# Performance work log

Measured on AMD Instinct MI355X. Metric: run time of the kernel, lower is better.

Reference implementation:

```python
import math
import jax, jax.numpy as jnp
import numpy as np

B, L, ENC_IN, TFEAT = 32, 1024, 21, 4
DM, EXP = 256, 2
DI = DM * EXP            # 512 d_inner
DST = 64                 # d_state (= configs.d_ff in this repo)
HD = 64                  # headdim
NH = DI // HD            # 8 heads
DC = 4                   # d_conv
NL = 4                   # n_layers
PRED = 192
CO = 21
Q = 64                   # SSD chunk length
DIP = 2 * DI + 2 * DST + NH    # in_proj out dim (z, xBC, dt)
CONVD = DI + 2 * DST           # depthwise-conv channels


def silu(x):
    return x * jax.nn.sigmoid(x)


def positional_embedding(l, d):
    pe = np.zeros((l, d), np.float32)
    pos = np.arange(l, dtype=np.float32)[:, None]
    div = np.exp(np.arange(0, d, 2, dtype=np.float32) * (-math.log(10000.0) / d))
    pe[:, 0::2] = np.sin(pos * div)
    pe[:, 1::2] = np.cos(pos * div)
    return jnp.asarray(pe)


def layernorm(x, g, b):
    m = jnp.mean(x, -1, keepdims=True)
    v = jnp.mean((x - m) ** 2, -1, keepdims=True)
    return (x - m) * jax.lax.rsqrt(v + 1e-5) * g + b


def segsum(x):
    # x: (..., T) -> (..., T, T); out[i,j] = sum_{j<k<=i} x[k], -inf above diagonal
    T = x.shape[-1]
    xx = jnp.broadcast_to(x[..., :, None], (*x.shape, T))
    m1 = jnp.tril(jnp.ones((T, T), bool), -1)
    xs = jnp.cumsum(jnp.where(m1, xx, 0.0), axis=-2)
    m2 = jnp.tril(jnp.ones((T, T), bool), 0)
    return jnp.where(m2, xs, -jnp.inf)


def ssd(X, A, Bm, Cm):
    # chunked SSD (Mamba2). X: (b,l,h,p) = x*dt; A: (b,l,h) = dt*(-exp(A_log)); B,C: (b,l,n)
    b, l, h, p = X.shape
    c = l // Q
    Xc = X.reshape(b, c, Q, h, p)
    Ac = A.reshape(b, c, Q, h).transpose(0, 3, 1, 2)      # (b,h,c,q)
    Bc = Bm.reshape(b, c, Q, -1)
    Cc = Cm.reshape(b, c, Q, -1)
    Acum = jnp.cumsum(Ac, -1)                              # (b,h,c,q)
    Lmat = jnp.exp(segsum(Ac))                             # (b,h,c,q,q)
    Y_diag = jnp.einsum('bcqn,bcsn,bhcqs,bcshp->bcqhp', Cc, Bc, Lmat, Xc)
    decay_states = jnp.exp(Acum[..., -1:] - Acum)          # (b,h,c,q)
    states = jnp.einsum('bcqn,bhcq,bcqhp->bchpn', Bc, decay_states, Xc)
    states = jnp.concatenate([jnp.zeros_like(states[:, :1]), states], axis=1)  # (b,c+1,h,p,n)
    decay_chunk = jnp.exp(segsum(jnp.pad(Acum[..., -1], ((0, 0), (0, 0), (1, 0)))))  # (b,h,c+1,c+1)
    new_states = jnp.einsum('bhzc,bchpn->bzhpn', decay_chunk, states)
    states = new_states[:, :-1]                            # (b,c,h,p,n) entering each chunk
    sdo = jnp.exp(Acum)                                    # (b,h,c,q)
    Y_off = jnp.einsum('bcqn,bchpn,bhcq->bcqhp', Cc, states, sdo)
    return (Y_diag + Y_off).reshape(b, l, h, p)


def mamba2(x, Wi, cw, cb, dtb, Alog, Dp, gw, Wo):
    b, l, _ = x.shape
    zxbcdt = x @ Wi.T                                      # (b,l,DIP)
    z = zxbcdt[..., :DI]
    xBC = zxbcdt[..., DI:DI + CONVD]
    dt = zxbcdt[..., DI + CONVD:]
    # causal depthwise conv (kernel DC) + SiLU
    xp = jnp.pad(xBC, ((0, 0), (DC - 1, 0), (0, 0)))
    xBC = silu(sum(xp[:, k:k + l, :] * cw[:, k] for k in range(DC)) + cb)
    xs = xBC[..., :DI].reshape(b, l, NH, HD)
    Bm = xBC[..., DI:DI + DST]
    Cm = xBC[..., DI + DST:]
    dt = jax.nn.softplus(dt + dtb)                         # (b,l,NH)
    A = -jnp.exp(Alog)                                     # (NH,)
    y = ssd(xs * dt[..., None], dt * A, Bm, Cm) + xs * Dp[:, None]
    y = y.reshape(b, l, DI)
    y = y * silu(z)                                        # gated RMSNorm
    y = y * jax.lax.rsqrt(jnp.mean(y * y, -1, keepdims=True) + 1e-5) * gw
    return y @ Wo.T


def setup_inputs():
    key = jax.random.key(0)
    ks = jax.random.split(key, 16)
    x_enc = jax.random.normal(ks[0], (B, L, ENC_IN), jnp.float32)
    x_mark_enc = jax.random.normal(ks[1], (B, L, TFEAT), jnp.float32)
    x_dec = jax.random.normal(ks[2], (B, 240, ENC_IN), jnp.float32)
    x_mark_dec = jax.random.normal(ks[3], (B, 240, TFEAT), jnp.float32)
    token_w = jax.random.normal(ks[4], (DM, ENC_IN, 3), jnp.float32) * 0.1
    temb_w = jax.random.normal(ks[5], (DM, TFEAT), jnp.float32) * 0.1
    ln_g = jnp.ones((NL, DM), jnp.float32)
    ln_b = jnp.zeros((NL, DM), jnp.float32)
    in_proj_w = jax.random.normal(ks[6], (NL, DIP, DM), jnp.float32) * (DM ** -0.5)
    conv_w = jax.random.normal(ks[7], (NL, CONVD, DC), jnp.float32) * 0.2
    conv_b = jnp.zeros((NL, CONVD), jnp.float32)
    dt_bias = jax.random.normal(ks[8], (NL, NH), jnp.float32) * 0.5
    A_log = jnp.log(jax.random.uniform(ks[9], (NL, NH), jnp.float32, 1.0, 16.0))
    Dskip = jnp.ones((NL, NH), jnp.float32)
    gnorm_w = jnp.ones((NL, DI), jnp.float32)
    out_proj_w = jax.random.normal(ks[10], (NL, DM, DI), jnp.float32) * (DI ** -0.5)
    head_w = jax.random.normal(ks[11], (CO, DM), jnp.float32) * (DM ** -0.5)
    return dict(x_enc=x_enc, x_mark_enc=x_mark_enc, x_dec=x_dec, x_mark_dec=x_mark_dec,
                token_w=token_w, temb_w=temb_w, ln_g=ln_g, ln_b=ln_b,
                in_proj_w=in_proj_w, conv_w=conv_w, conv_b=conv_b, dt_bias=dt_bias,
                A_log=A_log, Dskip=Dskip, gnorm_w=gnorm_w, out_proj_w=out_proj_w,
                head_w=head_w)


def reference(x_enc, x_mark_enc, x_dec, x_mark_dec, token_w, temb_w, ln_g, ln_b,
              in_proj_w, conv_w, conv_b, dt_bias, A_log, Dskip, gnorm_w, out_proj_w, head_w):
    # instance normalization (detached stats)
    mean = jax.lax.stop_gradient(jnp.mean(x_enc, 1, keepdims=True))
    xz = x_enc - mean
    std = jax.lax.stop_gradient(jnp.sqrt(jnp.var(xz, axis=1, keepdims=True) + 1e-5))
    xz = xz / std
    l = xz.shape[1]
    # token embedding: circular-pad Conv1d(enc_in->d_model, k=3)
    xpad = jnp.pad(xz, ((0, 0), (1, 1), (0, 0)), mode='wrap')
    tok = sum(jnp.einsum('blc,dc->bld', xpad[:, k:k + l], token_w[:, :, k]) for k in range(3))
    h = tok + positional_embedding(l, DM)[None] + x_mark_enc @ temb_w.T
    for i in range(NL):
        y = mamba2(h, in_proj_w[i], conv_w[i], conv_b[i], dt_bias[i], A_log[i],
                   Dskip[i], gnorm_w[i], out_proj_w[i])
        h = layernorm(h + y, ln_g[i], ln_b[i])
    out = h @ head_w.T
    out = out * std + mean
    return out[:, -PRED:, :]
```

## Files before the change

### kernel.cpp

```cpp
#include <hip/hip_runtime.h>
#include <hip/hip_bf16.h>


typedef unsigned short ushort_t;
typedef unsigned int uint_t;
typedef __attribute__((ext_vector_type(8))) short short8;
typedef __attribute__((ext_vector_type(4))) float f32x4;
typedef __attribute__((ext_vector_type(4))) ushort_t ushort4_t;

__device__ __forceinline__ float b2f(ushort_t u) {
    uint_t v = ((uint_t)u) << 16;
    return __builtin_bit_cast(float, v);
}
__device__ __forceinline__ ushort_t f2b(float f) {
    uint_t u = __builtin_bit_cast(uint_t, f);
    uint_t r = (u + 0x7FFFu + ((u >> 16) & 1u)) >> 16;
    return (ushort_t)r;
}
__device__ __forceinline__ float silu_f(float x) {
    return x / (1.f + __expf(-x));
}
__device__ __forceinline__ void gl_lds16(const ushort_t* g, ushort_t* l) {
    __builtin_amdgcn_global_load_lds(
        (const __attribute__((address_space(1))) unsigned int*)g,
        (__attribute__((address_space(3))) unsigned int*)l, 16, 0, 0);
}

__global__ __launch_bounds__(256) void cvt_pad_ip(const float* __restrict__ in,
        ushort_t* __restrict__ out) {
    int i = blockIdx.x * 256 + threadIdx.x;
    if (i >= 4 * 1280 * 256) return;
    int layer = i / (1280 * 256);
    int rem = i - layer * 1280 * 256;
    int n = rem >> 8, k = rem & 255;
    out[i] = (n < 1160) ? f2b(in[(size_t)layer * 1160 * 256 + n * 256 + k]) : (ushort_t)0;
}
__global__ __launch_bounds__(256) void cvt_wop(const float* __restrict__ in,
        const float* __restrict__ gw, ushort_t* __restrict__ out) {
    int i = blockIdx.x * 256 + threadIdx.x;
    int layer = i >> 17;
    int c = i & 511;
    out[i] = f2b(in[i] * gw[layer * 512 + c]);
}
__global__ __launch_bounds__(256) void cvt_convw(const float* __restrict__ in,
        float* __restrict__ out) {
    int i = blockIdx.x * 256 + threadIdx.x;
    if (i >= 10240) return;
    int layer = i / 2560;
    int rem = i - layer * 2560;
    int k = rem / 640, ch = rem - k * 640;
    out[i] = in[layer * 2560 + ch * 4 + k];
}

__global__ __launch_bounds__(256) void pe_kernel(float* __restrict__ pe) {
    int l = blockIdx.x, d = threadIdx.x;
    float div = __expf((float)(d & ~1) * (-9.210340371976184f / 256.0f));
    float arg = (float)l * div;
    pe[l * 256 + d] = (d & 1) ? cosf(arg) : sinf(arg);
}

__global__ __launch_bounds__(256) void stats_kernel(const float* __restrict__ xe,
        float* __restrict__ meanb, float* __restrict__ stdb, float* __restrict__ rstdb) {
    int bi = blockIdx.x;
    int b = bi / 21, c = bi - b * 21;
    int tid = threadIdx.x;
    float s = 0.f, s2 = 0.f;
    for (int l = tid; l < 1024; l += 256) {
        float v = xe[(b * 1024 + l) * 21 + c];
        s += v; s2 += v * v;
    }
    __shared__ float r1[4], r2[4];
    for (int o = 32; o > 0; o >>= 1) { s += __shfl_down(s, o, 64); s2 += __shfl_down(s2, o, 64); }
    if ((tid & 63) == 0) { r1[tid >> 6] = s; r2[tid >> 6] = s2; }
    __syncthreads();
    if (tid == 0) {
        float S = r1[0] + r1[1] + r1[2] + r1[3];
        float S2 = r2[0] + r2[1] + r2[2] + r2[3];
        float m = S * (1.f / 1024.f);
        float var = S2 * (1.f / 1024.f) - m * m;
        float sd = sqrtf(var + 1e-5f);
        meanb[bi] = m; stdb[bi] = sd; rstdb[bi] = 1.f / sd;
    }
}

__global__ __launch_bounds__(256) void embed3_kernel(const float* __restrict__ xe,
        const float* __restrict__ xm, const float* __restrict__ tokw,
        const float* __restrict__ tembw, const float* __restrict__ pe,
        const float* __restrict__ meanb, const float* __restrict__ rstdb,
        float* __restrict__ h, ushort_t* __restrict__ hbf) {
    int blk = blockIdx.x;
    int b = blk >> 4, t = blk & 15;
    int l0 = t * 64;
    int tid = threadIdx.x;
    __shared__ float xw[66][22];
    __shared__ float xmw[64][4];
    __shared__ float mn[21], rs[21];
    if (tid < 21) { mn[tid] = meanb[b * 21 + tid]; rs[tid] = rstdb[b * 21 + tid]; }
    float twr[63];
    {
        const float* tp = tokw + tid * 63;
        #pragma unroll
        for (int i = 0; i < 63; i++) twr[i] = tp[i];
    }
    float tbr[4];
    #pragma unroll
    for (int k = 0; k < 4; k++) tbr[k] = tembw[tid * 4 + k];
    __syncthreads();
    for (int i = tid; i < 1386; i += 256) {
        int row = i / 21, c = i - row * 21;
        int gl = (l0 - 1 + row + 1024) & 1023;
        xw[row][c] = (xe[(size_t)(b * 1024 + gl) * 21 + c] - mn[c]) * rs[c];
    }
    {
        int row = tid >> 2, c = tid & 3;
        xmw[row][c] = xm[(size_t)(b * 1024 + l0 + row) * 4 + c];
    }
    __syncthreads();
    int d = tid;
    float acc2 = 0.f, acc1 = 0.f;
    for (int r = 0; r < 66; r++) {
        float s0 = 0.f, s1 = 0.f, s2 = 0.f;
        #pragma unroll
        for (int c = 0; c < 21; c++) {
            float xv = xw[r][c];
            s0 += xv * twr[c * 3 + 0];
            s1 += xv * twr[c * 3 + 1];
            s2 += xv * twr[c * 3 + 2];
        }
        if (r >= 2) {
            int li = r - 2;
            float acc = acc2 + s2 + pe[(size_t)(l0 + li) * 256 + d];
            #pragma unroll
            for (int k = 0; k < 4; k++) acc += xmw[li][k] * tbr[k];
            size_t o = (size_t)(b * 1024 + l0 + li) * 256 + d;
            h[o] = acc;
            hbf[o] = f2b(acc);
        }
        acc2 = acc1 + s1;
        acc1 = s0;
    }
}

template<int KDIM>
__device__ __forceinline__ void gemm128_main(const ushort_t* __restrict__ Ab,
        const ushort_t* __restrict__ Wb, ushort_t* sA, ushort_t* sW,
        f32x4 (&acc)[16], int m0, int n0) {
    int tid = threadIdx.x;
    int w = tid >> 6, lane = tid & 63;
    int wm = w >> 1, wn = w & 1;
    int rr = lane & 15, quad = lane >> 4;
    int srow0 = w * 32 + (lane >> 2);
    int skk = (lane & 3) * 8;
    int sl0 = w * 1024 + lane * 8;
    for (int k0 = 0; k0 < KDIM; k0 += 64) {
        __syncthreads();
        #pragma unroll
        for (int p = 0; p < 2; p++) {
            #pragma unroll
            for (int j = 0; j < 2; j++) {
                int row = srow0 + j * 16;
                int koff = k0 + p * 32 + skk;
                gl_lds16(Ab + (size_t)(m0 + row) * KDIM + koff, &sA[p * 4096 + sl0 + j * 512]);
                gl_lds16(Wb + (size_t)(n0 + row) * KDIM + koff, &sW[p * 4096 + sl0 + j * 512]);
            }
        }
        __syncthreads();
        #pragma unroll
        for (int p = 0; p < 2; p++) {
            short8 a[4], b[4];
            #pragma unroll
            for (int i = 0; i < 4; i++)
                a[i] = *(const short8*)&sA[p * 4096 + (wm * 64 + i * 16 + rr) * 32 + quad * 8];
            #pragma unroll
            for (int j = 0; j < 4; j++)
                b[j] = *(const short8*)&sW[p * 4096 + (wn * 64 + j * 16 + rr) * 32 + quad * 8];
            #pragma unroll
            for (int i = 0; i < 4; i++)
                #pragma unroll
                for (int j = 0; j < 4; j++)
                    acc[i * 4 + j] = __builtin_amdgcn_mfma_f32_16x16x32_bf16(a[i], b[j], acc[i * 4 + j], 0, 0, 0);
        }
    }
}

__global__ __launch_bounds__(256) void gemm_ip(const ushort_t* __restrict__ A,
        const ushort_t* __restrict__ W, ushort_t* __restrict__ zbuf,
        ushort_t* __restrict__ xbuf) {
    int blk = blockIdx.x;
    int tm = blk / 10, tn = blk - tm * 10;
    int m0 = tm * 128, n0 = tn * 128;
    __shared__ ushort_t sA[8192], sW[8192];
    f32x4 acc[16];
    #pragma unroll
    for (int i = 0; i < 16; i++) acc[i] = (f32x4){0.f, 0.f, 0.f, 0.f};
    gemm128_main<256>(A, W, sA, sW, acc, m0, n0);
    int lane = threadIdx.x & 63, w = threadIdx.x >> 6;
    int wm = w >> 1, wn = w & 1;
    int rr = lane & 15, quad = lane >> 4;
    #pragma unroll
    for (int i = 0; i < 4; i++) {
        int mrow = m0 + wm * 64 + i * 16 + quad * 4;
        #pragma unroll
        for (int j = 0; j < 4; j++) {
            int n = n0 + wn * 64 + j * 16 + rr;
            #pragma unroll
            for (int r2 = 0; r2 < 4; r2++) {
                ushort_t v = f2b(acc[i * 4 + j][r2]);
                if (n < 512) zbuf[(size_t)(mrow + r2) * 512 + n] = v;
                else if (n < 1160) xbuf[(size_t)(mrow + r2) * 704 + (n - 512)] = v;
            }
        }
    }
}

__global__ __launch_bounds__(256) void gemm_og(const ushort_t* __restrict__ Yb,
        const ushort_t* __restrict__ Zb, const ushort_t* __restrict__ Wb,
        float* __restrict__ h, ushort_t* __restrict__ hbf,
        const float* __restrict__ lng, const float* __restrict__ lnb) {
    int m0 = blockIdx.x * 64;
    int tid = threadIdx.x;
    int w = tid >> 6, lane = tid & 63;
    int wm = w >> 1, wn = w & 1;
    int rr = lane & 15, quad = lane >> 4;
    __shared__ ushort_t sA[4096];
    __shared__ ushort_t sW[16384];
    __shared__ float gssq[64];
    __shared__ float rsum[64][2], rssq[64][2];

    int arow = tid >> 2;
    int akq = (tid & 3) * 16;
    const ushort_t* yrow = Yb + (size_t)(m0 + arow) * 512 + akq;
    const ushort_t* zrow = Zb + (size_t)(m0 + arow) * 512 + akq;
    ushort_t* adst = &sA[((tid & 3) >> 1) * 2048 + arow * 32 + (tid & 1) * 16];

    f32x4 acc[2][8];
    #pragma unroll
    for (int i = 0; i < 2; i++)
        #pragma unroll
        for (int j = 0; j < 8; j++) acc[i][j] = (f32x4){0.f, 0.f, 0.f, 0.f};
    float ssqr = 0.f;

    short8 y0 = *(const short8*)(yrow);
    short8 y1 = *(const short8*)(yrow + 8);
    short8 z0 = *(const short8*)(zrow);
    short8 z1 = *(const short8*)(zrow + 8);

    for (int k0 = 0; k0 < 512; k0 += 64) {
        __syncthreads();
        short8 ga, gb;
        #pragma unroll
        for (int jj = 0; jj < 8; jj++) {
            float g = b2f(((ushort_t*)&y0)[jj]) * silu_f(b2f(((ushort_t*)&z0)[jj]));
            ssqr += g * g;
            ((ushort_t*)&ga)[jj] = f2b(g);
        }
        #pragma unroll
        for (int jj = 0; jj < 8; jj++) {
            float g = b2f(((ushort_t*)&y1)[jj]) * silu_f(b2f(((ushort_t*)&z1)[jj]));
            ssqr += g * g;
            ((ushort_t*)&gb)[jj] = f2b(g);
        }
        *(short8*)adst = ga;
        *(short8*)(adst + 8) = gb;
        if (k0 + 64 < 512) {
            y0 = *(const short8*)(yrow + k0 + 64);
            y1 = *(const short8*)(yrow + k0 + 72);
            z0 = *(const short8*)(zrow + k0 + 64);
            z1 = *(const short8*)(zrow + k0 + 72);
        }
        #pragma unroll
        for (int p = 0; p < 2; p++) {
            #pragma unroll
            for (int j = 0; j < 4; j++)
                gl_lds16(Wb + (size_t)(w * 64 + j * 16 + (lane >> 2)) * 512
                             + k0 + p * 32 + (lane & 3) * 8,
                         &sW[p * 8192 + w * 2048 + j * 512 + lane * 8]);
        }
        __syncthreads();
        #pragma unroll
        for (int p = 0; p < 2; p++) {
            short8 a[2], b[8];
            #pragma unroll
            for (int i = 0; i < 2; i++)
                a[i] = *(const short8*)&sA[p * 2048 + (wm * 32 + i * 16 + rr) * 32 + quad * 8];
            #pragma unroll
            for (int j = 0; j < 8; j++)
                b[j] = *(const short8*)&sW[p * 8192 + (wn * 128 + j * 16 + rr) * 32 + quad * 8];
            #pragma unroll
            for (int i = 0; i < 2; i++)
                #pragma unroll
                for (int j = 0; j < 8; j++)
                    acc[i][j] = __builtin_amdgcn_mfma_f32_16x16x32_bf16(a[i], b[j], acc[i][j], 0, 0, 0);
        }
    }

    ssqr += __shfl_xor(ssqr, 1, 64);
    ssqr += __shfl_xor(ssqr, 2, 64);
    if ((tid & 3) == 0) gssq[arow] = ssqr;
    __syncthreads();

    float gl[8], bl[8];
    #pragma unroll
    for (int j = 0; j < 8; j++) {
        int col = wn * 128 + j * 16 + rr;
        gl[j] = lng[col]; bl[j] = lnb[col];
    }
    #pragma unroll
    for (int i = 0; i < 2; i++) {
        #pragma unroll
        for (int r2 = 0; r2 < 4; r2++) {
            int rowl = wm * 32 + i * 16 + quad * 4 + r2;
            float rmsv = rsqrtf(gssq[rowl] * (1.f / 512.f) + 1e-5f);
            size_t gbase = (size_t)(m0 + rowl) * 256;
            float s = 0.f, s2 = 0.f;
            #pragma unroll
            for (int j = 0; j < 8; j++) {
                int col = wn * 128 + j * 16 + rr;
                float xv = h[gbase + col] + acc[i][j][r2] * rmsv;
                acc[i][j][r2] = xv;
                s += xv; s2 += xv * xv;
            }
            #pragma unroll
            for (int o = 1; o < 16; o <<= 1) {
                s += __shfl_xor(s, o, 64);
                s2 += __shfl_xor(s2, o, 64);
            }
            if (rr == 0) { rsum[rowl][wn] = s; rssq[rowl][wn] = s2; }
        }
    }
    __syncthreads();
    #pragma unroll
    for (int i = 0; i < 2; i++) {
        #pragma unroll
        for (int r2 = 0; r2 < 4; r2++) {
            int rowl = wm * 32 + i * 16 + quad * 4 + r2;
            float S = rsum[rowl][0] + rsum[rowl][1];
            float S2 = rssq[rowl][0] + rssq[rowl][1];
            float mu = S * (1.f / 256.f);
            float var = S2 * (1.f / 256.f) - mu * mu;
            float rstd = rsqrtf(var + 1e-5f);
            size_t gbase = (size_t)(m0 + rowl) * 256;
            #pragma unroll
            for (int j = 0; j < 8; j++) {
                int col = wn * 128 + j * 16 + rr;
                float o = (acc[i][j][r2] - mu) * rstd * gl[j] + bl[j];
                h[gbase + col] = o;
                hbf[gbase + col] = f2b(o);
            }
        }
    }
}

__global__ __launch_bounds__(256) void conv_kernel(const ushort_t* __restrict__ xbuf,
        const float* __restrict__ cwt, const float* __restrict__ cb,
        const float* __restrict__ dtb, ushort_t* __restrict__ xc,
        float* __restrict__ dts) {
    if (blockIdx.x >= 2560) {
        int r = (blockIdx.x - 2560) * 256 + threadIdx.x;
        short8 dv = *(const short8*)(xbuf + (size_t)r * 704 + 640);
        #pragma unroll
        for (int j = 0; j < 8; j++) {
            float x = b2f(((ushort_t*)&dv)[j]) + dtb[j];
            dts[(size_t)r * 8 + j] = (x > 20.f) ? x : log1pf(__expf(x));
        }
        return;
    }
    int idx = blockIdx.x * 256 + threadIdx.x;
    int g = idx % 80;
    int rt = idx / 80;
    int ch0 = g * 8;
    int b = rt >> 8;
    int l0 = (rt & 255) << 2;
    float wgt[4][8];
    #pragma unroll
    for (int k = 0; k < 4; k++) {
        float4 w0 = *(const float4*)(cwt + k * 640 + ch0);
        float4 w1 = *(const float4*)(cwt + k * 640 + ch0 + 4);
        wgt[k][0] = w0.x; wgt[k][1] = w0.y; wgt[k][2] = w0.z; wgt[k][3] = w0.w;
        wgt[k][4] = w1.x; wgt[k][5] = w1.y; wgt[k][6] = w1.z; wgt[k][7] = w1.w;
    }
    float bias[8];
    {
        float4 b0 = *(const float4*)(cb + ch0);
        float4 b1 = *(const float4*)(cb + ch0 + 4);
        bias[0] = b0.x; bias[1] = b0.y; bias[2] = b0.z; bias[3] = b0.w;
        bias[4] = b1.x; bias[5] = b1.y; bias[6] = b1.z; bias[7] = b1.w;
    }
    short8 xr[7];
    const ushort_t* base = xbuf + (size_t)(b * 1024 + l0) * 704 + ch0;
    #pragma unroll
    for (int i = 0; i < 7; i++) {
        int ll = l0 - 3 + i;
        if (ll >= 0) xr[i] = *(const short8*)(base + (ptrdiff_t)(i - 3) * 704);
        else         xr[i] = (short8){0, 0, 0, 0, 0, 0, 0, 0};
    }
    #pragma unroll
    for (int lo = 0; lo < 4; lo++) {
        float acc[8];
        #pragma unroll
        for (int j = 0; j < 8; j++) acc[j] = bias[j];
        #pragma unroll
        for (int k = 0; k < 4; k++) {
            #pragma unroll
            for (int j = 0; j < 8; j++)
                acc[j] += b2f(((ushort_t*)&xr[lo + k])[j]) * wgt[k][j];
        }
        short8 o;
        #pragma unroll
        for (int j = 0; j < 8; j++) ((ushort_t*)&o)[j] = f2b(silu_f(acc[j]));
        *(short8*)(xc + (size_t)(b * 1024 + l0 + lo) * 640 + ch0) = o;
    }
}

__global__ __launch_bounds__(256) void ssd_stateA4(const ushort_t* __restrict__ xc,
        const float* __restrict__ dts, const float* __restrict__ alog,
        float* __restrict__ stbuf, float* __restrict__ acbuf) {
    int idx = blockIdx.x;
    int bh = idx >> 2, grp = idx & 3;
    int b = bh >> 3, h = bh & 7;
    float Ah = -__expf(alog[h]);
    int tid = threadIdx.x;
    int q = tid >> 2, pb = (tid & 3) * 16;
    int w = tid >> 6, lane = tid & 63;
    int rr = lane & 15, quad = lane >> 4, qb = w * 16;

    __shared__ ushort_t Bt[64][72], Xt[64][72];
    __shared__ float dec_s[64];
    __shared__ float ad_sh;

    float T[4][4];
    #pragma unroll
    for (int t = 0; t < 4; t++)
        #pragma unroll
        for (int r2 = 0; r2 < 4; r2++) T[t][r2] = 0.f;

    ushort_t bv[16], xv[16];
    float d_pf = 0.f;
    {
        int chunk = grp * 4;
        int l0 = chunk * 64;
        const ushort_t* xrow = xc + (size_t)(b * 1024 + l0 + q) * 640;
        *(short8*)&bv[0] = *(const short8*)(xrow + 512 + pb);
        *(short8*)&bv[8] = *(const short8*)(xrow + 512 + pb + 8);
        *(short8*)&xv[0] = *(const short8*)(xrow + h * 64 + pb);
        *(short8*)&xv[8] = *(const short8*)(xrow + h * 64 + pb + 8);
        if (tid < 64)
            d_pf = dts[(size_t)(b * 1024 + l0 + tid) * 8 + h];
    }

    for (int c4 = 0; c4 < 4; c4++) {
        int chunk = grp * 4 + c4;
        size_t cidx = (size_t)bh * 16 + chunk;
        #pragma unroll
        for (int j = 0; j < 16; j++) Xt[pb + j][q] = xv[j];
        if (tid < 64) {
            float d = d_pf;
            float a = d * Ah;
            #pragma unroll
            for (int off = 1; off < 64; off <<= 1) {
                float t = __shfl_up(a, off, 64);
                if (tid >= off) a += t;
            }
            acbuf[cidx * 64 + tid] = a;
            float tot = __shfl(a, 63, 64);
            dec_s[tid] = __expf(tot - a) * d;
            if (tid == 0) ad_sh = __expf(tot);
        }
        __syncthreads();
        {
            float dq = dec_s[q];
            #pragma unroll
            for (int j = 0; j < 16; j++) Bt[pb + j][q] = f2b(b2f(bv[j]) * dq);
        }
        if (c4 < 3) {
            int l0n = (chunk + 1) * 64;
            const ushort_t* xrow = xc + (size_t)(b * 1024 + l0n + q) * 640;
            *(short8*)&bv[0] = *(const short8*)(xrow + 512 + pb);
            *(short8*)&bv[8] = *(const short8*)(xrow + 512 + pb + 8);
            *(short8*)&xv[0] = *(const short8*)(xrow + h * 64 + pb);
            *(short8*)&xv[8] = *(const short8*)(xrow + h * 64 + pb + 8);
            if (tid < 64)
                d_pf = dts[(size_t)(b * 1024 + l0n + tid) * 8 + h];
        }
        __syncthreads();
        f32x4 acc[4];
        #pragma unroll
        for (int t = 0; t < 4; t++) acc[t] = (f32x4){0.f, 0.f, 0.f, 0.f};
        #pragma unroll
        for (int ks = 0; ks < 2; ks++) {
            short8 a = *(const short8*)(&Bt[qb + rr][ks * 32 + quad * 8]);
            #pragma unroll
            for (int t = 0; t < 4; t++) {
                short8 bb = *(const short8*)(&Xt[t * 16 + rr][ks * 32 + quad * 8]);
                acc[t] = __builtin_amdgcn_mfma_f32_16x16x32_bf16(a, bb, acc[t], 0, 0, 0);
            }
        }
        {
            float ad = ad_sh;
            #pragma unroll
            for (int t = 0; t < 4; t++)
                #pragma unroll
                for (int r2 = 0; r2 < 4; r2++)
                    T[t][r2] = ad * T[t][r2] + acc[t][r2];
        }
        __syncthreads();
    }
    float* sb = stbuf + (size_t)idx * 4096;
    #pragma unroll
    for (int t = 0; t < 4; t++) {
        int p = t * 16 + rr;
        #pragma unroll
        for (int r2 = 0; r2 < 4; r2++)
            sb[(qb + quad * 4 + r2) * 64 + p] = T[t][r2];
    }
}

__global__ __launch_bounds__(256) void ssd_scan(const float* __restrict__ stbuf,
        const float* __restrict__ acbuf, float* __restrict__ gst) {
    int bh = blockIdx.x >> 2, sl = blockIdx.x & 3;
    int tid = threadIdx.x;
    size_t boff = (size_t)sl * 1024 + tid * 4;
    float4 S = make_float4(0.f, 0.f, 0.f, 0.f);
    for (int g = 0; g < 4; g++) {
        *(float4*)(gst + (size_t)(bh * 4 + g) * 4096 + boff) = S;
        float Ag = 1.f;
        #pragma unroll
        for (int c = 0; c < 4; c++)
            Ag *= __expf(acbuf[((size_t)bh * 16 + g * 4 + c) * 64 + 63]);
        float4 v = *(const float4*)(stbuf + (size_t)(bh * 4 + g) * 4096 + boff);
        S.x = Ag * S.x + v.x; S.y = Ag * S.y + v.y;
        S.z = Ag * S.z + v.z; S.w = Ag * S.w + v.w;
    }
}

__global__ __launch_bounds__(256) void ssd_outBC4(const ushort_t* __restrict__ xc,
        const float* __restrict__ dts, const float* __restrict__ acbuf,
        const float* __restrict__ dsk, const float* __restrict__ gst,
        ushort_t* __restrict__ ybuf) {
    int idx = blockIdx.x;
    int bh = idx >> 2, grp = idx & 3;
    int b = bh >> 3, h = bh & 7;
    float Dh = dsk[h];
    int tid = threadIdx.x;
    int q = tid >> 2, pb = (tid & 3) * 16;
    int w = tid >> 6, lane = tid & 63;
    int rr = lane & 15, quad = lane >> 4, qb = w * 16;

    __shared__ ushort_t Cs[64][68], Bs[64][68], Xt[64][68], Gs[64][68],
                        Bt[64][68], Shi[64][68], Slo[64][68];
    __shared__ float acum_s[64], dtq_s[64], ea_s[64], dec_s[64];
    __shared__ float ad_sh;

    float S[4][4];
    {
        const float* s0 = gst + (size_t)idx * 4096;
        #pragma unroll
        for (int t = 0; t < 4; t++) {
            int p = t * 16 + rr;
            #pragma unroll
            for (int r2 = 0; r2 < 4; r2++)
                S[t][r2] = s0[(qb + quad * 4 + r2) * 64 + p];
        }
    }

    ushort_t bv[16], cv[16], xv[16];
    float a_pf = 0.f, d_pf = 0.f;
    {
        int chunk = grp * 4;
        int l0 = chunk * 64;
        const ushort_t* xrow = xc + (size_t)(b * 1024 + l0 + q) * 640;
        *(short8*)&bv[0] = *(const short8*)(xrow + 512 + pb);
        *(short8*)&bv[8] = *(const short8*)(xrow + 512 + pb + 8);
        *(short8*)&cv[0] = *(const short8*)(xrow + 576 + pb);
        *(short8*)&cv[8] = *(const short8*)(xrow + 576 + pb + 8);
        *(short8*)&xv[0] = *(const short8*)(xrow + h * 64 + pb);
        *(short8*)&xv[8] = *(const short8*)(xrow + h * 64 + pb + 8);
        if (tid < 64) {
            size_t cidx = (size_t)bh * 16 + chunk;
            a_pf = acbuf[cidx * 64 + tid];
            d_pf = dts[(size_t)(b * 1024 + l0 + tid) * 8 + h];
        }
    }

    for (int c4 = 0; c4 < 4; c4++) {
        int chunk = grp * 4 + c4;
        int l0 = chunk * 64;
        *(short8*)&Bs[q][pb]     = *(const short8*)&bv[0];
        *(short8*)&Bs[q][pb + 8] = *(const short8*)&bv[8];
        *(short8*)&Cs[q][pb]     = *(const short8*)&cv[0];
        *(short8*)&Cs[q][pb + 8] = *(const short8*)&cv[8];
        #pragma unroll
        for (int j = 0; j < 16; j++) Xt[pb + j][q] = xv[j];
        if (tid < 64) {
            float a = a_pf;
            acum_s[tid] = a;
            ea_s[tid] = __expf(a);
            float d = d_pf;
            dtq_s[tid] = d;
            float tot = __shfl(a, 63, 64);
            dec_s[tid] = __expf(tot - a) * d;
            if (tid == 0) ad_sh = __expf(tot);
        }
        #pragma unroll
        for (int t = 0; t < 4; t++) {
            int p = t * 16 + rr;
            #pragma unroll
            for (int r2 = 0; r2 < 4; r2++) {
                float s = S[t][r2];
                ushort_t hi = f2b(s);
                Shi[p][qb + quad * 4 + r2] = hi;
                Slo[p][qb + quad * 4 + r2] = f2b(s - b2f(hi));
            }
        }
        __syncthreads();

        {
            float dq = dec_s[q];
            #pragma unroll
            for (int j = 0; j < 16; j++)
                Bt[pb + j][q] = f2b(b2f(bv[j]) * dq);
        }
        if (c4 < 3) {
            int l0n = (chunk + 1) * 64;
            const ushort_t* xrow = xc + (size_t)(b * 1024 + l0n + q) * 640;
            *(short8*)&bv[0] = *(const short8*)(xrow + 512 + pb);
            *(short8*)&bv[8] = *(const short8*)(xrow + 512 + pb + 8);
            *(short8*)&cv[0] = *(const short8*)(xrow + 576 + pb);
            *(short8*)&cv[8] = *(const short8*)(xrow + 576 + pb + 8);
            *(short8*)&xv[0] = *(const short8*)(xrow + h * 64 + pb);
            *(short8*)&xv[8] = *(const short8*)(xrow + h * 64 + pb + 8);
            if (tid < 64) {
                size_t cidxn = (size_t)bh * 16 + chunk + 1;
                a_pf = acbuf[cidxn * 64 + tid];
                d_pf = dts[(size_t)(b * 1024 + l0n + tid) * 8 + h];
            }
        }
        {
            f32x4 g[4];
            #pragma unroll
            for (int t = 0; t < 4; t++) g[t] = (f32x4){0.f, 0.f, 0.f, 0.f};
            #pragma unroll
            for (int ks = 0; ks < 2; ks++) {
                short8 a = *(const short8*)(&Cs[qb + rr][ks * 32 + quad * 8]);
                #pragma unroll
                for (int t = 0; t < 4; t++) {
                    short8 bb = *(const short8*)(&Bs[t * 16 + rr][ks * 32 + quad * 8]);
                    g[t] = __builtin_amdgcn_mfma_f32_16x16x32_bf16(a, bb, g[t], 0, 0, 0);
                }
            }
            #pragma unroll
            for (int t = 0; t < 4; t++) {
                int s = t * 16 + rr;
                float as = acum_s[s], dss = dtq_s[s];
                #pragma unroll
                for (int r2 = 0; r2 < 4; r2++) {
                    int qq = qb + quad * 4 + r2;
                    float v = (s <= qq) ? g[t][r2] * __expf(acum_s[qq] - as) * dss : 0.f;
                    Gs[qq][s] = f2b(v);
                }
            }
        }
        __syncthreads();

        f32x4 aD[4], aO[4];
        #pragma unroll
        for (int t = 0; t < 4; t++) { aD[t] = (f32x4){0.f,0.f,0.f,0.f}; aO[t] = (f32x4){0.f,0.f,0.f,0.f}; }
        #pragma unroll
        for (int ks = 0; ks < 2; ks++) {
            short8 ga = *(const short8*)(&Gs[qb + rr][ks * 32 + quad * 8]);
            short8 ca = *(const short8*)(&Cs[qb + rr][ks * 32 + quad * 8]);
            #pragma unroll
            for (int t = 0; t < 4; t++) {
                short8 xb = *(const short8*)(&Xt[t * 16 + rr][ks * 32 + quad * 8]);
                short8 sh = *(const short8*)(&Shi[t * 16 + rr][ks * 32 + quad * 8]);
                short8 sl = *(const short8*)(&Slo[t * 16 + rr][ks * 32 + quad * 8]);
                aD[t] = __builtin_amdgcn_mfma_f32_16x16x32_bf16(ga, xb, aD[t], 0, 0, 0);
                aO[t] = __builtin_amdgcn_mfma_f32_16x16x32_bf16(ca, sh, aO[t], 0, 0, 0);
                aO[t] = __builtin_amdgcn_mfma_f32_16x16x32_bf16(ca, sl, aO[t], 0, 0, 0);
            }
        }
        {
            f32x4 acc[4];
            #pragma unroll
            for (int t = 0; t < 4; t++) acc[t] = (f32x4){0.f, 0.f, 0.f, 0.f};
            #pragma unroll
            for (int ks = 0; ks < 2; ks++) {
                short8 a = *(const short8*)(&Bt[qb + rr][ks * 32 + quad * 8]);
                #pragma unroll
                for (int t = 0; t < 4; t++) {
                    short8 bb = *(const short8*)(&Xt[t * 16 + rr][ks * 32 + quad * 8]);
                    acc[t] = __builtin_amdgcn_mfma_f32_16x16x32_bf16(a, bb, acc[t], 0, 0, 0);
                }
            }
            #pragma unroll
            for (int t = 0; t < 4; t++) {
                int p = t * 16 + rr;
                #pragma unroll
                for (int r2 = 0; r2 < 4; r2++) {
                    int qq = qb + quad * 4 + r2;
                    float y = aD[t][r2] + ea_s[qq] * aO[t][r2] + Dh * b2f(Xt[p][qq]);
                    ybuf[(size_t)(b * 1024 + l0 + qq) * 512 + h * 64 + p] = f2b(y);
                }
            }
            float ad = ad_sh;
            #pragma unroll
            for (int t = 0; t < 4; t++)
                #pragma unroll
                for (int r2 = 0; r2 < 4; r2++)
                    S[t][r2] = ad * S[t][r2] + acc[t][r2];
        }
        __syncthreads();
    }
}

__global__ __launch_bounds__(256) void head_kernel(const float* __restrict__ h,
        const float* __restrict__ hw, const float* __restrict__ stdb,
        const float* __restrict__ meanb, float* __restrict__ out) {
    int blk = blockIdx.x;
    int b = blk / 192, t = blk - b * 192;
    int l = 832 + t;
    int tid = threadIdx.x;
    __shared__ float hr[256];
    hr[tid] = h[(size_t)(b * 1024 + l) * 256 + tid];
    __syncthreads();
    if (tid < 21) {
        float acc = 0.f;
        for (int k = 0; k < 256; k++) acc += hr[k] * hw[tid * 256 + k];
        out[(size_t)blk * 21 + tid] = acc * stdb[b * 21 + tid] + meanb[b * 21 + tid];
    }
}

extern "C" void kernel_launch(void* const* d_in, const int* in_sizes, int n_in,
                              void* d_out, int out_size, void* d_ws, size_t ws_size,
                              hipStream_t stream) {
    const float* x_enc  = (const float*)d_in[0];
    const float* x_mark = (const float*)d_in[1];
    const float* tokw   = (const float*)d_in[4];
    const float* tembw  = (const float*)d_in[5];
    const float* ln_g   = (const float*)d_in[6];
    const float* ln_b   = (const float*)d_in[7];
    const float* ipw    = (const float*)d_in[8];
    const float* cw     = (const float*)d_in[9];
    const float* cb     = (const float*)d_in[10];
    const float* dtb    = (const float*)d_in[11];
    const float* alog   = (const float*)d_in[12];
    const float* dsk    = (const float*)d_in[13];
    const float* gw     = (const float*)d_in[14];
    const float* opw    = (const float*)d_in[15];
    const float* hw     = (const float*)d_in[16];
    float* out = (float*)d_out;

    char* w = (char*)d_ws;
    size_t off = 0;
    auto alloc = [&](size_t bytes) -> void* {
        void* p = w + off;
        off += (bytes + 255) & ~(size_t)255;
        return p;
    };
    float* meanb  = (float*)alloc(672 * 4);
    float* stdb   = (float*)alloc(672 * 4);
    float* rstdb  = (float*)alloc(672 * 4);
    float* dts    = (float*)alloc((size_t)262144 * 4);
    float* pebuf  = (float*)alloc((size_t)262144 * 4);
    float* cwt    = (float*)alloc((size_t)10240 * 4);
    float* hbuf   = (float*)alloc((size_t)8388608 * 4);
    ushort_t* hbf = (ushort_t*)alloc((size_t)8388608 * 2);
    ushort_t* zbuf= (ushort_t*)alloc((size_t)32768 * 512 * 2);
    ushort_t* xc  = (ushort_t*)alloc((size_t)32768 * 640 * 2);
    char* R       = (char*)alloc((size_t)71303168);
    ushort_t* ybuf= (ushort_t*)alloc((size_t)32768 * 512 * 2);
    ushort_t* wipb= (ushort_t*)alloc((size_t)4 * 1280 * 256 * 2);
    ushort_t* wopb= (ushort_t*)alloc((size_t)4 * 256 * 512 * 2);
    ushort_t* xbuf = (ushort_t*)R;
    float* stbuf   = (float*)R;
    float* acbuf   = (float*)(R + 67108864);
    float* gst     = (float*)hbf;
    (void)ws_size; (void)in_sizes; (void)n_in; (void)out_size;

    stats_kernel<<<672, 256, 0, stream>>>(x_enc, meanb, stdb, rstdb);
    pe_kernel<<<1024, 256, 0, stream>>>(pebuf);
    cvt_pad_ip<<<5120, 256, 0, stream>>>(ipw, wipb);
    cvt_wop<<<2048, 256, 0, stream>>>(opw, gw, wopb);
    cvt_convw<<<40, 256, 0, stream>>>(cw, cwt);
    embed3_kernel<<<512, 256, 0, stream>>>(x_enc, x_mark, tokw, tembw, pebuf,
                                           meanb, rstdb, hbuf, hbf);

    for (int layer = 0; layer < 4; layer++) {
        gemm_ip<<<2560, 256, 0, stream>>>(hbf, wipb + (size_t)layer * 1280 * 256,
                                          zbuf, xbuf);
        conv_kernel<<<2688, 256, 0, stream>>>(xbuf, cwt + layer * 2560,
                                              cb + layer * 640, dtb + layer * 8,
                                              xc, dts);
        ssd_stateA4<<<1024, 256, 0, stream>>>(xc, dts, alog + layer * 8, stbuf, acbuf);
        ssd_scan<<<1024, 256, 0, stream>>>(stbuf, acbuf, gst);
        ssd_outBC4<<<1024, 256, 0, stream>>>(xc, dts, acbuf, dsk + layer * 8,
                                             gst, ybuf);
        gemm_og<<<512, 256, 0, stream>>>(ybuf, zbuf,
                                         wopb + (size_t)layer * 256 * 512,
                                         hbuf, hbf,
                                         ln_g + layer * 256, ln_b + layer * 256);
    }

    head_kernel<<<6144, 256, 0, stream>>>(hbuf, hw, stdb, meanb, out);
}
```

Measured before the change: 780.6 us.

## Fuse inter-group state scan into SSD output kernel and swizzle in_proj GEMM tiles per XCD

New measurement: 741.8 us. -5.0%, faster.

```diff
diff --git a/kernel.cpp b/kernel.cpp
--- a/kernel.cpp
+++ b/kernel.cpp
@@ -186,8 +186,11 @@
 __global__ __launch_bounds__(256) void gemm_ip(const ushort_t* __restrict__ A,
         const ushort_t* __restrict__ W, ushort_t* __restrict__ zbuf,
         ushort_t* __restrict__ xbuf) {
-    int blk = blockIdx.x;
-    int tm = blk / 10, tn = blk - tm * 10;
+    int g = blockIdx.x;
+    int xcd = g & 7, s = g >> 3;
+    int sq = s / 10;
+    int tn = s - sq * 10;
+    int tm = (sq << 3) | xcd;
     int m0 = tm * 128, n0 = tn * 128;
     __shared__ ushort_t sA[8192], sW[8192];
     f32x4 acc[16];
@@ -515,27 +518,9 @@
     }
 }
 
-__global__ __launch_bounds__(256) void ssd_scan(const float* __restrict__ stbuf,
-        const float* __restrict__ acbuf, float* __restrict__ gst) {
-    int bh = blockIdx.x >> 2, sl = blockIdx.x & 3;
-    int tid = threadIdx.x;
-    size_t boff = (size_t)sl * 1024 + tid * 4;
-    float4 S = make_float4(0.f, 0.f, 0.f, 0.f);
-    for (int g = 0; g < 4; g++) {
-        *(float4*)(gst + (size_t)(bh * 4 + g) * 4096 + boff) = S;
-        float Ag = 1.f;
-        #pragma unroll
-        for (int c = 0; c < 4; c++)
-            Ag *= __expf(acbuf[((size_t)bh * 16 + g * 4 + c) * 64 + 63]);
-        float4 v = *(const float4*)(stbuf + (size_t)(bh * 4 + g) * 4096 + boff);
-        S.x = Ag * S.x + v.x; S.y = Ag * S.y + v.y;
-        S.z = Ag * S.z + v.z; S.w = Ag * S.w + v.w;
-    }
-}
-
 __global__ __launch_bounds__(256) void ssd_outBC4(const ushort_t* __restrict__ xc,
         const float* __restrict__ dts, const float* __restrict__ acbuf,
-        const float* __restrict__ dsk, const float* __restrict__ gst,
+        const float* __restrict__ dsk, const float* __restrict__ stbuf,
         ushort_t* __restrict__ ybuf) {
     int idx = blockIdx.x;
     int bh = idx >> 2, grp = idx & 3;
@@ -552,14 +537,22 @@
     __shared__ float ad_sh;
 
     float S[4][4];
-    {
-        const float* s0 = gst + (size_t)idx * 4096;
+    #pragma unroll
+    for (int t = 0; t < 4; t++)
+        #pragma unroll
+        for (int r2 = 0; r2 < 4; r2++) S[t][r2] = 0.f;
+    for (int g = 0; g < grp; g++) {
+        float Ag = 1.f;
+        #pragma unroll
+        for (int c = 0; c < 4; c++)
+            Ag *= __expf(acbuf[((size_t)bh * 16 + g * 4 + c) * 64 + 63]);
+        const float* s0 = stbuf + (size_t)(bh * 4 + g) * 4096;
         #pragma unroll
         for (int t = 0; t < 4; t++) {
             int p = t * 16 + rr;
             #pragma unroll
             for (int r2 = 0; r2 < 4; r2++)
-                S[t][r2] = s0[(qb + quad * 4 + r2) * 64 + p];
+                S[t][r2] = Ag * S[t][r2] + s0[(qb + quad * 4 + r2) * 64 + p];
         }
     }
 
@@ -774,7 +767,6 @@
     ushort_t* xbuf = (ushort_t*)R;
     float* stbuf   = (float*)R;
     float* acbuf   = (float*)(R + 67108864);
-    float* gst     = (float*)hbf;
     (void)ws_size; (void)in_sizes; (void)n_in; (void)out_size;
 
     stats_kernel<<<672, 256, 0, stream>>>(x_enc, meanb, stdb, rstdb);
@@ -792,9 +784,8 @@
                                               cb + layer * 640, dtb + layer * 8,
                                               xc, dts);
         ssd_stateA4<<<1024, 256, 0, stream>>>(xc, dts, alog + layer * 8, stbuf, acbuf);
-        ssd_scan<<<1024, 256, 0, stream>>>(stbuf, acbuf, gst);
         ssd_outBC4<<<1024, 256, 0, stream>>>(xc, dts, acbuf, dsk + layer * 8,
-                                             gst, ybuf);
+                                             stbuf, ybuf);
         gemm_og<<<512, 256, 0, stream>>>(ybuf, zbuf,
                                          wopb + (size_t)layer * 256 * 512,
                                          hbuf, hbf,
```
